# Optimization experiments

Measured on AMD Instinct MI355X. Metric: run time of the kernel, lower is better.

## Reference

```python
import jax, jax.numpy as jnp
import numpy as np

LN_EPS = 1e-5


def _layernorm(x, w, b):
    mu = jnp.mean(x, axis=-1, keepdims=True)
    var = jnp.mean((x - mu) ** 2, axis=-1, keepdims=True)
    return (x - mu) * jax.lax.rsqrt(var + LN_EPS) * w + b


def setup_inputs() -> dict:
    key = jax.random.key(0)
    n, d = 512, 256
    ks = jax.random.split(key, 12)
    s = 1.0 / np.sqrt(d)
    inp = {
        "h": jax.random.normal(ks[0], (n, d), dtype=jnp.float32),
        "e": jax.random.normal(ks[1], (n, n, d), dtype=jnp.float32),
        "t_emb": jax.random.normal(ks[2], (d,), dtype=jnp.float32),
        "W1": jax.random.uniform(ks[3], (d, d), jnp.float32, -s, s),
        "W2": jax.random.uniform(ks[4], (d, d), jnp.float32, -s, s),
        "W3": jax.random.uniform(ks[5], (d, d), jnp.float32, -s, s),
        "W_t": jax.random.uniform(ks[6], (d, d), jnp.float32, -s, s),
        "W4": jax.random.uniform(ks[7], (d, d), jnp.float32, -s, s),
        "W5": jax.random.uniform(ks[8], (d, d), jnp.float32, -s, s),
        "gate_w": jax.random.uniform(ks[9], (d, 1), jnp.float32, -s, s),
        "gate_b": jax.random.uniform(ks[10], (1,), jnp.float32, -s, s),
        "ln_e_w": jnp.ones((d,), jnp.float32),
        "ln_e_b": jnp.zeros((d,), jnp.float32),
        "ln_h_w": jnp.ones((d,), jnp.float32),
        "ln_h_b": jnp.zeros((d,), jnp.float32),
    }
    return inp


def reference(h, e, t_emb, W1, W2, W3, W_t, W4, W5, gate_w, gate_b,
              ln_e_w, ln_e_b, ln_h_w, ln_h_b):
    # nn.Linear applies x @ W.T (no bias except gate)
    t_bias = t_emb @ W_t.T                      # (d,)
    hi = (h @ W1.T)[:, None, :]                 # (n,1,d)
    hj = (h @ W2.T)[None, :, :]                 # (1,n,d)
    pre = hi + hj + jnp.einsum('ijd,kd->ijk', e, W3) + t_bias  # (n,n,d)
    e_new = jax.nn.relu(_layernorm(pre, ln_e_w, ln_e_b))       # (n,n,d)
    logits = e_new @ gate_w + gate_b            # (n,n,1)
    eta = jax.nn.softmax(logits, axis=1)        # softmax over j (dim=1)
    agg = jnp.einsum('ijk,ijd,kd->ik', eta * 1.0, e_new, W5) if False else \
          jnp.sum(eta * jnp.einsum('ijd,kd->ijk', e_new, W5), axis=1)  # (n,d)
    h_new = h + jax.nn.relu(_layernorm(h @ W4.T + agg, ln_h_w, ln_h_b))
    return (h_new, e_new)
```

## Files before the change

### kernel.cpp

```cpp
#include <hip/hip_runtime.h>

#define NN 512
#define DD 256

typedef float f32x4 __attribute__((ext_vector_type(4)));
typedef short s16x8 __attribute__((ext_vector_type(8)));

__device__ __forceinline__ unsigned short f2bf(float f) {
    unsigned u = __float_as_uint(f);
    u += 0x7fffu + ((u >> 16) & 1u);
    return (unsigned short)(u >> 16);
}

__global__ __launch_bounds__(256) void k1_pre(
    const float* __restrict__ h,  const float* __restrict__ W1,
    const float* __restrict__ W2, const float* __restrict__ W4,
    const float* __restrict__ t_emb, const float* __restrict__ W_t,
    const float* __restrict__ W3,
    float* __restrict__ hb, float* __restrict__ hW2, float* __restrict__ hW4,
    unsigned short* __restrict__ w3b)
{
    __shared__ float xs[8][DD];
    __shared__ float st[DD];
    const int b = blockIdx.x;
    const int t = threadIdx.x;
    if (b < 64) {
        #pragma unroll
        for (int r = 0; r < 8; ++r) xs[r][t] = h[(size_t)(b * 8 + r) * DD + t];
        st[t] = t_emb[t];
        __syncthreads();
        float a1[8], a2[8], a4[8];
        #pragma unroll
        for (int r = 0; r < 8; ++r) { a1[r] = 0.f; a2[r] = 0.f; a4[r] = 0.f; }
        float tb = 0.f;
        for (int d = 0; d < DD; ++d) {
            const float w1 = W1[(size_t)t * DD + d];
            const float w2 = W2[(size_t)t * DD + d];
            const float w4 = W4[(size_t)t * DD + d];
            tb = fmaf(st[d], W_t[(size_t)t * DD + d], tb);
            #pragma unroll
            for (int r = 0; r < 8; ++r) {
                const float x = xs[r][d];
                a1[r] = fmaf(x, w1, a1[r]);
                a2[r] = fmaf(x, w2, a2[r]);
                a4[r] = fmaf(x, w4, a4[r]);
            }
        }
        #pragma unroll
        for (int r = 0; r < 8; ++r) {
            const size_t o = (size_t)(b * 8 + r) * DD + t;
            hb[o] = a1[r] + tb; hW2[o] = a2[r]; hW4[o] = a4[r];
        }
    } else {
        for (int c = t; c < DD * DD / 4; c += 256) {
            const f32x4 v = *reinterpret_cast<const f32x4*>(W3 + (size_t)c * 4);
            const unsigned lo = ((unsigned)f2bf(v[1]) << 16) | f2bf(v[0]);
            const unsigned hi = ((unsigned)f2bf(v[3]) << 16) | f2bf(v[2]);
            *reinterpret_cast<uint2*>(w3b + (size_t)c * 4) = make_uint2(lo, hi);
        }
    }
}

__global__ __launch_bounds__(256) void k2_big(
    const float* __restrict__ e,
    const unsigned short* __restrict__ w3b,
    const float* __restrict__ hb, const float* __restrict__ hW2,
    const float* __restrict__ gate_w, const float* __restrict__ gate_b,
    const float* __restrict__ ln_e_w, const float* __restrict__ ln_e_b,
    float* __restrict__ out_e, float* __restrict__ logits)
{
    const int row_base = blockIdx.x * 32;
    const int i = row_base >> 9;
    const int tid = threadIdx.x;
    const int w = tid >> 6;
    const int l = tid & 63;
    const int l15 = l & 15;
    const int lg = l >> 4;

    __shared__ __align__(16) unsigned char sA[32 * 256 * 2];
    __shared__ float s_part[32][4][2];
    __shared__ float s_mu[32];
    __shared__ float s_rs[32];
    __shared__ float s_glog[32][4];

    const float* src = e + (size_t)row_base * DD;
    f32x4 av[8];
    #pragma unroll
    for (int s = 0; s < 8; ++s)
        av[s] = *reinterpret_cast<const f32x4*>(src + (size_t)(s * 256 + tid) * 4);

    const unsigned short* bp = w3b + (size_t)(w * 64 + l15) * DD + lg * 8;
    s16x8 bcur[4];
    #pragma unroll
    for (int n = 0; n < 4; ++n)
        bcur[n] = *reinterpret_cast<const s16x8*>(bp + (size_t)n * 16 * DD);

    #pragma unroll
    for (int s = 0; s < 8; ++s) {
        const int flat = s * 256 + tid;
        const int r = flat >> 6;
        const int c4 = (flat & 63) * 4;
        const f32x4 v = av[s];
        const unsigned lo = ((unsigned)f2bf(v[1]) << 16) | f2bf(v[0]);
        const unsigned hi = ((unsigned)f2bf(v[3]) << 16) | f2bf(v[2]);
        const unsigned byte = ((unsigned)(r * 512 + c4 * 2)) ^ ((unsigned)(r & 7) << 4);
        *reinterpret_cast<uint2*>(sA + byte) = make_uint2(lo, hi);
    }
    __syncthreads();

    f32x4 acc[2][4];
    #pragma unroll
    for (int m = 0; m < 2; ++m)
        #pragma unroll
        for (int n = 0; n < 4; ++n)
            acc[m][n] = (f32x4){0.f, 0.f, 0.f, 0.f};

    const unsigned aswz = ((unsigned)(l15 & 7) << 4);
    #pragma unroll
    for (int kk = 0; kk < 8; ++kk) {
        s16x8 bnxt[4];
        if (kk < 7) {
            #pragma unroll
            for (int n = 0; n < 4; ++n)
                bnxt[n] = *reinterpret_cast<const s16x8*>(bp + (size_t)n * 16 * DD + (kk + 1) * 32);
        }
        s16x8 afr[2];
        #pragma unroll
        for (int m = 0; m < 2; ++m) {
            const unsigned byte = ((unsigned)((m * 16 + l15) * 512 + kk * 64 + lg * 16)) ^ aswz;
            afr[m] = *reinterpret_cast<const s16x8*>(sA + byte);
        }
        #pragma unroll
        for (int n = 0; n < 4; ++n)
            #pragma unroll
            for (int m = 0; m < 2; ++m)
                acc[m][n] = __builtin_amdgcn_mfma_f32_16x16x32_bf16(afr[m], bcur[n], acc[m][n], 0, 0, 0);
        if (kk < 7) {
            #pragma unroll
            for (int n = 0; n < 4; ++n) bcur[n] = bnxt[n];
        }
    }

    float hbn[4], lnwc[4], lnbc[4], gwc[4];
    #pragma unroll
    for (int n = 0; n < 4; ++n) {
        const int col = w * 64 + n * 16 + l15;
        hbn[n]  = hb[(size_t)i * DD + col];
        lnwc[n] = ln_e_w[col];
        lnbc[n] = ln_e_b[col];
        gwc[n]  = gate_w[col];
    }

    #pragma unroll
    for (int m = 0; m < 2; ++m) {
        #pragma unroll
        for (int q = 0; q < 4; ++q) {
            const int r = m * 16 + lg * 4 + q;
            const int j = (row_base + r) & 511;
            const float* h2p = hW2 + (size_t)j * DD + w * 64 + l15;
            float s1 = 0.f, s2 = 0.f;
            #pragma unroll
            for (int n = 0; n < 4; ++n) {
                float v = acc[m][n][q] + hbn[n] + h2p[n * 16];
                acc[m][n][q] = v;
                s1 += v;
                s2 = fmaf(v, v, s2);
            }
            #pragma unroll
            for (int s = 1; s < 16; s <<= 1) {
                s1 += __shfl_xor(s1, s, 64);
                s2 += __shfl_xor(s2, s, 64);
            }
            if (l15 == 0) { s_part[r][w][0] = s1; s_part[r][w][1] = s2; }
        }
    }
    __syncthreads();
    if (tid < 32) {
        float S1 = 0.f, S2 = 0.f;
        #pragma unroll
        for (int ww = 0; ww < 4; ++ww) { S1 += s_part[tid][ww][0]; S2 += s_part[tid][ww][1]; }
        const float mu = S1 * (1.f / 256.f);
        const float var = S2 * (1.f / 256.f) - mu * mu;
        s_mu[tid] = mu;
        s_rs[tid] = rsqrtf(var + 1e-5f);
    }
    __syncthreads();

    #pragma unroll
    for (int m = 0; m < 2; ++m) {
        #pragma unroll
        for (int q = 0; q < 4; ++q) {
            const int r = m * 16 + lg * 4 + q;
            const float mu = s_mu[r];
            const float rs = s_rs[r];
            const size_t rowg = (size_t)(row_base + r);
            float gl = 0.f;
            #pragma unroll
            for (int n = 0; n < 4; ++n) {
                const int col = w * 64 + n * 16 + l15;
                float v = (acc[m][n][q] - mu) * rs * lnwc[n] + lnbc[n];
                v = fmaxf(v, 0.f);
                out_e[rowg * DD + col] = v;
                gl = fmaf(v, gwc[n], gl);
            }
            #pragma unroll
            for (int s = 1; s < 16; s <<= 1) gl += __shfl_xor(gl, s, 64);
            if (l15 == 0) s_glog[r][w] = gl;
        }
    }
    __syncthreads();
    if (tid < 32) {
        float g = gate_b[0];
        #pragma unroll
        for (int ww = 0; ww < 4; ++ww) g += s_glog[tid][ww];
        logits[(size_t)row_base + tid] = g;
    }
}

__global__ __launch_bounds__(256) void k3_soft(
    const float* __restrict__ logits, const float* __restrict__ out_e,
    float* __restrict__ weighted)
{
    const int i = blockIdx.x;
    const int t = threadIdx.x;
    const int w = t >> 6;
    const int l = t & 63;
    __shared__ float seta[NN];
    __shared__ float red[256];
    __shared__ float red2[4][DD];

    const float l0 = logits[(size_t)i * NN + t];
    const float l1 = logits[(size_t)i * NN + 256 + t];

    red[t] = fmaxf(l0, l1);
    __syncthreads();
    for (int s = 128; s > 0; s >>= 1) {
        if (t < s) red[t] = fmaxf(red[t], red[t + s]);
        __syncthreads();
    }
    const float mx = red[0];
    __syncthreads();

    const float e0 = expf(l0 - mx);
    const float e1 = expf(l1 - mx);
    red[t] = e0 + e1;
    __syncthreads();
    for (int s = 128; s > 0; s >>= 1) {
        if (t < s) red[t] += red[t + s];
        __syncthreads();
    }
    const float inv = 1.f / red[0];
    seta[t] = e0 * inv;
    seta[256 + t] = e1 * inv;
    __syncthreads();

    const float* base = out_e + (size_t)i * NN * DD;
    f32x4 a0 = (f32x4){0.f, 0.f, 0.f, 0.f};
    f32x4 a1v = (f32x4){0.f, 0.f, 0.f, 0.f};
    for (int j0 = 0; j0 < NN; j0 += 8) {
        const int ja = j0 + w;
        const int jb = j0 + 4 + w;
        const float ea = seta[ja];
        const float eb = seta[jb];
        const f32x4 va = *reinterpret_cast<const f32x4*>(base + (size_t)ja * DD + l * 4);
        const f32x4 vb = *reinterpret_cast<const f32x4*>(base + (size_t)jb * DD + l * 4);
        #pragma unroll
        for (int q = 0; q < 4; ++q) {
            a0[q] = fmaf(ea, va[q], a0[q]);
            a1v[q] = fmaf(eb, vb[q], a1v[q]);
        }
    }
    #pragma unroll
    for (int q = 0; q < 4; ++q) a0[q] += a1v[q];
    *reinterpret_cast<f32x4*>(&red2[w][l * 4]) = a0;
    __syncthreads();
    weighted[(size_t)i * DD + t] = red2[0][t] + red2[1][t] + red2[2][t] + red2[3][t];
}

__global__ __launch_bounds__(256) void k4_final(
    const float* __restrict__ weighted, const float* __restrict__ W5,
    const float* __restrict__ hW4, const float* __restrict__ h,
    const float* __restrict__ ln_h_w, const float* __restrict__ ln_h_b,
    float* __restrict__ out_h)
{
    const int i = blockIdx.x;
    const int k = threadIdx.x;
    __shared__ float xs[DD];
    __shared__ float red[256];

    xs[k] = weighted[(size_t)i * DD + k];
    __syncthreads();
    float a = 0.f;
    for (int d = 0; d < DD; ++d) a = fmaf(xs[d], W5[(size_t)k * DD + d], a);
    const float p = hW4[(size_t)i * DD + k] + a;

    red[k] = p;
    __syncthreads();
    for (int s = 128; s > 0; s >>= 1) {
        if (k < s) red[k] += red[k + s];
        __syncthreads();
    }
    const float mu = red[0] * (1.f / 256.f);
    __syncthreads();
    const float d0 = p - mu;
    red[k] = d0 * d0;
    __syncthreads();
    for (int s = 128; s > 0; s >>= 1) {
        if (k < s) red[k] += red[k + s];
        __syncthreads();
    }
    const float rs = rsqrtf(red[0] * (1.f / 256.f) + 1e-5f);
    float v = d0 * rs * ln_h_w[k] + ln_h_b[k];
    v = fmaxf(v, 0.f);
    out_h[(size_t)i * DD + k] = h[(size_t)i * DD + k] + v;
}

extern "C" void kernel_launch(void* const* d_in, const int* in_sizes, int n_in,
                              void* d_out, int out_size, void* d_ws, size_t ws_size,
                              hipStream_t stream)
{
    const float* h      = (const float*)d_in[0];
    const float* e      = (const float*)d_in[1];
    const float* t_emb  = (const float*)d_in[2];
    const float* W1     = (const float*)d_in[3];
    const float* W2     = (const float*)d_in[4];
    const float* W3     = (const float*)d_in[5];
    const float* W_t    = (const float*)d_in[6];
    const float* W4     = (const float*)d_in[7];
    const float* W5     = (const float*)d_in[8];
    const float* gate_w = (const float*)d_in[9];
    const float* gate_b = (const float*)d_in[10];
    const float* ln_e_w = (const float*)d_in[11];
    const float* ln_e_b = (const float*)d_in[12];
    const float* ln_h_w = (const float*)d_in[13];
    const float* ln_h_b = (const float*)d_in[14];

    float* out_h = (float*)d_out;
    float* out_e = out_h + NN * DD;

    float* wsf      = (float*)d_ws;
    float* hb       = wsf;
    float* hW2      = hb + NN * DD;
    float* hW4      = hW2 + NN * DD;
    float* logits   = hW4 + NN * DD;
    float* weighted = logits + NN * NN;
    unsigned short* w3b = (unsigned short*)(weighted + NN * DD);

    k1_pre<<<65, 256, 0, stream>>>(h, W1, W2, W4, t_emb, W_t, W3,
                                   hb, hW2, hW4, w3b);
    k2_big<<<8192, 256, 0, stream>>>(e, w3b, hb, hW2, gate_w, gate_b,
                                     ln_e_w, ln_e_b, out_e, logits);
    k3_soft<<<512, 256, 0, stream>>>(logits, out_e, weighted);
    k4_final<<<512, 256, 0, stream>>>(weighted, W5, hW4, h, ln_h_w, ln_h_b, out_h);
}
```

Before: 325.4 us.

## Fuse softmax-weighted aggregation into edge kernel and prefetch next row tile

The edge GEMM+LayerNorm kernel now processes four 32-row tiles per block. It computes unnormalised exp(logit) weights and accumulates the weighted sum of e_new in registers, writing per-block partial sums and partition sums. A small reduce kernel then normalises them, so the separate softmax pass that re-read the full 256 MB out_e tensor is gone. The next tile's e rows are loaded while the current tile is being normalised. Softmax no longer subtracts the row max, which risks overflow for large logits, and the grid has four times fewer blocks.

Measured after the change: 346.6 us. 6.5% more time.

```diff
diff --git a/kernel.cpp b/kernel.cpp
--- a/kernel.cpp
+++ b/kernel.cpp
@@ -67,78 +67,31 @@
     const float* __restrict__ hb, const float* __restrict__ hW2,
     const float* __restrict__ gate_w, const float* __restrict__ gate_b,
     const float* __restrict__ ln_e_w, const float* __restrict__ ln_e_b,
-    float* __restrict__ out_e, float* __restrict__ logits)
-{
-    const int row_base = blockIdx.x * 32;
-    const int i = row_base >> 9;
+    float* __restrict__ out_e,
+    float* __restrict__ ws_part, float* __restrict__ ws_z)
+{
+    const int b = blockIdx.x;
+    const int row0 = b * 128;
+    const int i = b >> 2;
     const int tid = threadIdx.x;
     const int w = tid >> 6;
     const int l = tid & 63;
     const int l15 = l & 15;
     const int lg = l >> 4;
 
-    __shared__ __align__(16) unsigned char sA[32 * 256 * 2];
+    __shared__ __align__(16) unsigned char sA[2][32 * 256 * 2];
     __shared__ float s_part[32][4][2];
     __shared__ float s_mu[32];
     __shared__ float s_rs[32];
+    __shared__ float s_exp[32];
     __shared__ float s_glog[32][4];
 
-    const float* src = e + (size_t)row_base * DD;
-    f32x4 av[8];
-    #pragma unroll
-    for (int s = 0; s < 8; ++s)
-        av[s] = *reinterpret_cast<const f32x4*>(src + (size_t)(s * 256 + tid) * 4);
-
-    const unsigned short* bp = w3b + (size_t)(w * 64 + l15) * DD + lg * 8;
-    s16x8 bcur[4];
-    #pragma unroll
-    for (int n = 0; n < 4; ++n)
-        bcur[n] = *reinterpret_cast<const s16x8*>(bp + (size_t)n * 16 * DD);
-
-    #pragma unroll
-    for (int s = 0; s < 8; ++s) {
-        const int flat = s * 256 + tid;
-        const int r = flat >> 6;
-        const int c4 = (flat & 63) * 4;
-        const f32x4 v = av[s];
-        const unsigned lo = ((unsigned)f2bf(v[1]) << 16) | f2bf(v[0]);
-        const unsigned hi = ((unsigned)f2bf(v[3]) << 16) | f2bf(v[2]);
-        const unsigned byte = ((unsigned)(r * 512 + c4 * 2)) ^ ((unsigned)(r & 7) << 4);
-        *reinterpret_cast<uint2*>(sA + byte) = make_uint2(lo, hi);
-    }
-    __syncthreads();
-
-    f32x4 acc[2][4];
-    #pragma unroll
-    for (int m = 0; m < 2; ++m)
-        #pragma unroll
-        for (int n = 0; n < 4; ++n)
-            acc[m][n] = (f32x4){0.f, 0.f, 0.f, 0.f};
-
-    const unsigned aswz = ((unsigned)(l15 & 7) << 4);
-    #pragma unroll
-    for (int kk = 0; kk < 8; ++kk) {
-        s16x8 bnxt[4];
-        if (kk < 7) {
-            #pragma unroll
-            for (int n = 0; n < 4; ++n)
-                bnxt[n] = *reinterpret_cast<const s16x8*>(bp + (size_t)n * 16 * DD + (kk + 1) * 32);
-        }
-        s16x8 afr[2];
-        #pragma unroll
-        for (int m = 0; m < 2; ++m) {
-            const unsigned byte = ((unsigned)((m * 16 + l15) * 512 + kk * 64 + lg * 16)) ^ aswz;
-            afr[m] = *reinterpret_cast<const s16x8*>(sA + byte);
-        }
-        #pragma unroll
-        for (int n = 0; n < 4; ++n)
-            #pragma unroll
-            for (int m = 0; m < 2; ++m)
-                acc[m][n] = __builtin_amdgcn_mfma_f32_16x16x32_bf16(afr[m], bcur[n], acc[m][n], 0, 0, 0);
-        if (kk < 7) {
-            #pragma unroll
-            for (int n = 0; n < 4; ++n) bcur[n] = bnxt[n];
-        }
+    f32x4 avf[8];
+    {
+        const float* src = e + (size_t)row0 * DD;
+        #pragma unroll
+        for (int s = 0; s < 8; ++s)
+            avf[s] = *reinterpret_cast<const f32x4*>(src + (size_t)(s * 256 + tid) * 4);
     }
 
     float hbn[4], lnwc[4], lnbc[4], gwc[4];
@@ -150,131 +103,184 @@
         lnbc[n] = ln_e_b[col];
         gwc[n]  = gate_w[col];
     }
+    const float gb = gate_b[0];
+
+    float p[4] = {0.f, 0.f, 0.f, 0.f};
+    float z_acc = 0.f;
+
+    const unsigned aswz = ((unsigned)(l15 & 7) << 4);
+    const unsigned short* bp = w3b + (size_t)(w * 64 + l15) * DD + lg * 8;
+
+    for (int t = 0; t < 4; ++t) {
+        const int cur = t & 1;
+        #pragma unroll
+        for (int s = 0; s < 8; ++s) {
+            const int flat = s * 256 + tid;
+            const int r = flat >> 6;
+            const int c4 = (flat & 63) * 4;
+            const f32x4 v = avf[s];
+            const unsigned lo = ((unsigned)f2bf(v[1]) << 16) | f2bf(v[0]);
+            const unsigned hi = ((unsigned)f2bf(v[3]) << 16) | f2bf(v[2]);
+            const unsigned byte = ((unsigned)(r * 512 + c4 * 2)) ^ ((unsigned)(r & 7) << 4);
+            *reinterpret_cast<uint2*>(sA[cur] + byte) = make_uint2(lo, hi);
+        }
+        __syncthreads();
+
+        s16x8 bcur[4];
+        #pragma unroll
+        for (int n = 0; n < 4; ++n)
+            bcur[n] = *reinterpret_cast<const s16x8*>(bp + (size_t)n * 16 * DD);
+
+        f32x4 acc[2][4];
+        #pragma unroll
+        for (int m = 0; m < 2; ++m)
+            #pragma unroll
+            for (int n = 0; n < 4; ++n)
+                acc[m][n] = (f32x4){0.f, 0.f, 0.f, 0.f};
+
+        #pragma unroll
+        for (int kk = 0; kk < 8; ++kk) {
+            s16x8 bnxt[4];
+            if (kk < 7) {
+                #pragma unroll
+                for (int n = 0; n < 4; ++n)
+                    bnxt[n] = *reinterpret_cast<const s16x8*>(bp + (size_t)n * 16 * DD + (kk + 1) * 32);
+            }
+            s16x8 afr[2];
+            #pragma unroll
+            for (int m = 0; m < 2; ++m) {
+                const unsigned byte = ((unsigned)((m * 16 + l15) * 512 + kk * 64 + lg * 16)) ^ aswz;
+                afr[m] = *reinterpret_cast<const s16x8*>(sA[cur] + byte);
+            }
+            #pragma unroll
+            for (int n = 0; n < 4; ++n)
+                #pragma unroll
+                for (int m = 0; m < 2; ++m)
+                    acc[m][n] = __builtin_amdgcn_mfma_f32_16x16x32_bf16(afr[m], bcur[n], acc[m][n], 0, 0, 0);
+            if (kk < 7) {
+                #pragma unroll
+                for (int n = 0; n < 4; ++n) bcur[n] = bnxt[n];
+            }
+        }
+
+        #pragma unroll
+        for (int m = 0; m < 2; ++m) {
+            #pragma unroll
+            for (int q = 0; q < 4; ++q) {
+                const int r = m * 16 + lg * 4 + q;
+                const int j = (row0 + t * 32 + r) & 511;
+                const float* h2p = hW2 + (size_t)j * DD + w * 64 + l15;
+                float s1 = 0.f, s2 = 0.f;
+                #pragma unroll
+                for (int n = 0; n < 4; ++n) {
+                    const float v = acc[m][n][q] + hbn[n] + h2p[n * 16];
+                    acc[m][n][q] = v;
+                    s1 += v;
+                    s2 = fmaf(v, v, s2);
+                }
+                #pragma unroll
+                for (int s = 1; s < 16; s <<= 1) {
+                    s1 += __shfl_xor(s1, s, 64);
+                    s2 += __shfl_xor(s2, s, 64);
+                }
+                if (l15 == 0) { s_part[r][w][0] = s1; s_part[r][w][1] = s2; }
+            }
+        }
+        __syncthreads();
+
+        if (t < 3) {
+            const float* srcn = e + (size_t)(row0 + (t + 1) * 32) * DD;
+            #pragma unroll
+            for (int s = 0; s < 8; ++s)
+                avf[s] = *reinterpret_cast<const f32x4*>(srcn + (size_t)(s * 256 + tid) * 4);
+        }
+
+        if (tid < 32) {
+            float S1 = 0.f, S2 = 0.f;
+            #pragma unroll
+            for (int ww = 0; ww < 4; ++ww) { S1 += s_part[tid][ww][0]; S2 += s_part[tid][ww][1]; }
+            const float mu = S1 * (1.f / 256.f);
+            const float var = S2 * (1.f / 256.f) - mu * mu;
+            s_mu[tid] = mu;
+            s_rs[tid] = rsqrtf(var + 1e-5f);
+        }
+        __syncthreads();
+
+        #pragma unroll
+        for (int m = 0; m < 2; ++m) {
+            #pragma unroll
+            for (int q = 0; q < 4; ++q) {
+                const int r = m * 16 + lg * 4 + q;
+                const float mu = s_mu[r];
+                const float rs = s_rs[r];
+                const size_t rowg = (size_t)(row0 + t * 32 + r);
+                float gl = 0.f;
+                #pragma unroll
+                for (int n = 0; n < 4; ++n) {
+                    float v = (acc[m][n][q] - mu) * rs * lnwc[n] + lnbc[n];
+                    v = fmaxf(v, 0.f);
+                    acc[m][n][q] = v;
+                    out_e[rowg * DD + n * 16 + w * 64 + l15] = v;
+                    gl = fmaf(v, gwc[n], gl);
+                }
+                #pragma unroll
+                for (int s = 1; s < 16; s <<= 1) gl += __shfl_xor(gl, s, 64);
+                if (l15 == 0) s_glog[r][w] = gl;
+            }
+        }
+        __syncthreads();
+
+        if (tid < 32) {
+            float lv = gb;
+            #pragma unroll
+            for (int ww = 0; ww < 4; ++ww) lv += s_glog[tid][ww];
+            const float ex = __expf(lv);
+            s_exp[tid] = ex;
+            float zz = ex;
+            #pragma unroll
+            for (int s = 1; s < 32; s <<= 1) zz += __shfl_xor(zz, s, 64);
+            if (tid == 0) z_acc += zz;
+        }
+        __syncthreads();
+
+        #pragma unroll
+        for (int m = 0; m < 2; ++m) {
+            #pragma unroll
+            for (int q = 0; q < 4; ++q) {
+                const float ex = s_exp[m * 16 + lg * 4 + q];
+                #pragma unroll
+                for (int n = 0; n < 4; ++n)
+                    p[n] = fmaf(ex, acc[m][n][q], p[n]);
+            }
+        }
+    }
 
     #pragma unroll
-    for (int m = 0; m < 2; ++m) {
-        #pragma unroll
-        for (int q = 0; q < 4; ++q) {
-            const int r = m * 16 + lg * 4 + q;
-            const int j = (row_base + r) & 511;
-            const float* h2p = hW2 + (size_t)j * DD + w * 64 + l15;
-            float s1 = 0.f, s2 = 0.f;
-            #pragma unroll
-            for (int n = 0; n < 4; ++n) {
-                float v = acc[m][n][q] + hbn[n] + h2p[n * 16];
-                acc[m][n][q] = v;
-                s1 += v;
-                s2 = fmaf(v, v, s2);
-            }
-            #pragma unroll
-            for (int s = 1; s < 16; s <<= 1) {
-                s1 += __shfl_xor(s1, s, 64);
-                s2 += __shfl_xor(s2, s, 64);
-            }
-            if (l15 == 0) { s_part[r][w][0] = s1; s_part[r][w][1] = s2; }
-        }
-    }
-    __syncthreads();
-    if (tid < 32) {
-        float S1 = 0.f, S2 = 0.f;
-        #pragma unroll
-        for (int ww = 0; ww < 4; ++ww) { S1 += s_part[tid][ww][0]; S2 += s_part[tid][ww][1]; }
-        const float mu = S1 * (1.f / 256.f);
-        const float var = S2 * (1.f / 256.f) - mu * mu;
-        s_mu[tid] = mu;
-        s_rs[tid] = rsqrtf(var + 1e-5f);
-    }
-    __syncthreads();
-
+    for (int n = 0; n < 4; ++n) {
+        p[n] += __shfl_xor(p[n], 16, 64);
+        p[n] += __shfl_xor(p[n], 32, 64);
+    }
+    if (lg == 0) {
+        #pragma unroll
+        for (int n = 0; n < 4; ++n)
+            ws_part[(size_t)b * DD + w * 64 + n * 16 + l15] = p[n];
+    }
+    if (tid == 0) ws_z[b] = z_acc;
+}
+
+__global__ __launch_bounds__(256) void k3_reduce(
+    const float* __restrict__ ws_part, const float* __restrict__ ws_z,
+    float* __restrict__ weighted)
+{
+    const int i = blockIdx.x;
+    const int k = threadIdx.x;
+    float s = 0.f, z = 0.f;
     #pragma unroll
-    for (int m = 0; m < 2; ++m) {
-        #pragma unroll
-        for (int q = 0; q < 4; ++q) {
-            const int r = m * 16 + lg * 4 + q;
-            const float mu = s_mu[r];
-            const float rs = s_rs[r];
-            const size_t rowg = (size_t)(row_base + r);
-            float gl = 0.f;
-            #pragma unroll
-            for (int n = 0; n < 4; ++n) {
-                const int col = w * 64 + n * 16 + l15;
-                float v = (acc[m][n][q] - mu) * rs * lnwc[n] + lnbc[n];
-                v = fmaxf(v, 0.f);
-                out_e[rowg * DD + col] = v;
-                gl = fmaf(v, gwc[n], gl);
-            }
-            #pragma unroll
-            for (int s = 1; s < 16; s <<= 1) gl += __shfl_xor(gl, s, 64);
-            if (l15 == 0) s_glog[r][w] = gl;
-        }
-    }
-    __syncthreads();
-    if (tid < 32) {
-        float g = gate_b[0];
-        #pragma unroll
-        for (int ww = 0; ww < 4; ++ww) g += s_glog[tid][ww];
-        logits[(size_t)row_base + tid] = g;
-    }
-}
-
-__global__ __launch_bounds__(256) void k3_soft(
-    const float* __restrict__ logits, const float* __restrict__ out_e,
-    float* __restrict__ weighted)
-{
-    const int i = blockIdx.x;
-    const int t = threadIdx.x;
-    const int w = t >> 6;
-    const int l = t & 63;
-    __shared__ float seta[NN];
-    __shared__ float red[256];
-    __shared__ float red2[4][DD];
-
-    const float l0 = logits[(size_t)i * NN + t];
-    const float l1 = logits[(size_t)i * NN + 256 + t];
-
-    red[t] = fmaxf(l0, l1);
-    __syncthreads();
-    for (int s = 128; s > 0; s >>= 1) {
-        if (t < s) red[t] = fmaxf(red[t], red[t + s]);
-        __syncthreads();
-    }
-    const float mx = red[0];
-    __syncthreads();
-
-    const float e0 = expf(l0 - mx);
-    const float e1 = expf(l1 - mx);
-    red[t] = e0 + e1;
-    __syncthreads();
-    for (int s = 128; s > 0; s >>= 1) {
-        if (t < s) red[t] += red[t + s];
-        __syncthreads();
-    }
-    const float inv = 1.f / red[0];
-    seta[t] = e0 * inv;
-    seta[256 + t] = e1 * inv;
-    __syncthreads();
-
-    const float* base = out_e + (size_t)i * NN * DD;
-    f32x4 a0 = (f32x4){0.f, 0.f, 0.f, 0.f};
-    f32x4 a1v = (f32x4){0.f, 0.f, 0.f, 0.f};
-    for (int j0 = 0; j0 < NN; j0 += 8) {
-        const int ja = j0 + w;
-        const int jb = j0 + 4 + w;
-        const float ea = seta[ja];
-        const float eb = seta[jb];
-        const f32x4 va = *reinterpret_cast<const f32x4*>(base + (size_t)ja * DD + l * 4);
-        const f32x4 vb = *reinterpret_cast<const f32x4*>(base + (size_t)jb * DD + l * 4);
-        #pragma unroll
-        for (int q = 0; q < 4; ++q) {
-            a0[q] = fmaf(ea, va[q], a0[q]);
-            a1v[q] = fmaf(eb, vb[q], a1v[q]);
-        }
-    }
-    #pragma unroll
-    for (int q = 0; q < 4; ++q) a0[q] += a1v[q];
-    *reinterpret_cast<f32x4*>(&red2[w][l * 4]) = a0;
-    __syncthreads();
-    weighted[(size_t)i * DD + t] = red2[0][t] + red2[1][t] + red2[2][t] + red2[3][t];
+    for (int t = 0; t < 4; ++t) {
+        s += ws_part[(size_t)(i * 4 + t) * DD + k];
+        z += ws_z[i * 4 + t];
+    }
+    weighted[(size_t)i * DD + k] = s / z;
 }
 
 __global__ __launch_bounds__(256) void k4_final(
@@ -342,14 +348,15 @@
     float* hb       = wsf;
     float* hW2      = hb + NN * DD;
     float* hW4      = hW2 + NN * DD;
-    float* logits   = hW4 + NN * DD;
-    float* weighted = logits + NN * NN;
+    float* ws_part  = hW4 + NN * DD;
+    float* ws_z     = ws_part + 2048 * DD;
+    float* weighted = ws_z + 2048;
     unsigned short* w3b = (unsigned short*)(weighted + NN * DD);
 
     k1_pre<<<65, 256, 0, stream>>>(h, W1, W2, W4, t_emb, W_t, W3,
                                    hb, hW2, hW4, w3b);
-    k2_big<<<8192, 256, 0, stream>>>(e, w3b, hb, hW2, gate_w, gate_b,
-                                     ln_e_w, ln_e_b, out_e, logits);
-    k3_soft<<<512, 256, 0, stream>>>(logits, out_e, weighted);
+    k2_big<<<2048, 256, 0, stream>>>(e, w3b, hb, hW2, gate_w, gate_b,
+                                     ln_e_w, ln_e_b, out_e, ws_part, ws_z);
+    k3_reduce<<<512, 256, 0, stream>>>(ws_part, ws_z, weighted);
     k4_final<<<512, 256, 0, stream>>>(weighted, W5, hW4, h, ln_h_w, ln_h_b, out_h);
 }
```
